# Kernel optimization log

Measured on AMD Instinct MI355X. Metric: run time of the kernel, lower is better.

Reference implementation:

```python
import jax, jax.numpy as jnp
import numpy as np
from itertools import permutations

B, T, J = 65536, 3, 10
W_ASSIGN = 1.0  # assignments_loss_weight
W_CAT = 1.0     # categorizer_loss_weight


def setup_inputs() -> dict:
    key = jax.random.key(0)
    k1, k2, k3, k4 = jax.random.split(key, 4)
    assignments = jax.random.uniform(k1, (B, T, J, J), dtype=jnp.float32)
    category = jax.random.uniform(k2, (B, T), dtype=jnp.float32)
    assignments_labels = jax.random.uniform(k3, (B, T, J, J), dtype=jnp.float32)
    category_labels = jax.random.uniform(k4, (B, T), dtype=jnp.float32)
    return {
        "assignments": assignments,
        "category": category,
        "assignments_labels": assignments_labels,
        "category_labels": category_labels,
    }


def _bce(p, y):
    # torch.nn.BCELoss clamps log terms at -100
    logp = jnp.clip(jnp.log(p), -100.0, None)
    log1mp = jnp.clip(jnp.log1p(-p), -100.0, None)
    return -(y * logp + (1.0 - y) * log1mp)


def reference(assignments, category, assignments_labels, category_labels):
    t = assignments.shape[1]
    perms = jnp.asarray(list(permutations(range(t))), dtype=jnp.int32)  # [P, T]
    # gather all permutations at once: [B, P, T, J, J]
    gathered = assignments[:, perms]
    # per-(event, perm) mean BCE vs labels broadcast over perm axis -> [B, P]
    losses = _bce(gathered, assignments_labels[:, None]).mean(axis=(2, 3, 4))
    batch_losses = losses.min(axis=1)          # [B]
    best = losses.argmin(axis=1)               # [B], first-min tie-break like torch's strict <
    best_perm = perms[best]                    # [B, T]
    permuted_category = jnp.take_along_axis(category, best_perm, axis=1)  # [B, T]
    assignments_loss = batch_losses.mean()
    category_loss = _bce(permuted_category, category_labels).mean()
    return W_ASSIGN * assignments_loss + W_CAT * category_loss
```

## Files before the change

kernel.cpp:

```cpp
#include <hip/hip_runtime.h>


#define CLIP2 (-144.26950408889634f)
#define LN2   (0.6931471805599453f)

__launch_bounds__(256)
__global__ void hybrid_pass1(const float* __restrict__ assign,
                             const float* __restrict__ cat,
                             const float* __restrict__ assign_lab,
                             const float* __restrict__ cat_lab,
                             float* __restrict__ ws, int B) {
    const int tid = blockIdx.x * blockDim.x + threadIdx.x;
    const int b   = tid >> 2;
    const int q   = threadIdx.x & 3;

    float lsum = 0.f;

    if (b < B) {
        const float* Abq = assign     + (size_t)b * 300 + 4 * q;
        const float* Ybq = assign_lab + (size_t)b * 300 + 4 * q;

        const float* cp = cat     + (size_t)b * 3;
        const float* gp = cat_lab + (size_t)b * 3;
        float cb0 = cp[0], cb1 = cp[1], cb2 = cp[2];
        float gb0 = gp[0], gb1 = gp[1], gb2 = gp[2];

        float dacc[3][3] = {{0.f,0.f,0.f},{0.f,0.f,0.f},{0.f,0.f,0.f}};
        float s1a[3]     = {0.f, 0.f, 0.f};

        auto do_chunk = [&](const float* Ap, const float* Yp) {
            float4 av[3], yv[3];
            #pragma unroll
            for (int t = 0; t < 3; ++t) {
                av[t] = *(const float4*)(Ap + t * 100);
                yv[t] = *(const float4*)(Yp + t * 100);
            }
            float d[3][4];
            #pragma unroll
            for (int t = 0; t < 3; ++t) {
                float a[4] = {av[t].x, av[t].y, av[t].z, av[t].w};
                #pragma unroll
                for (int c = 0; c < 4; ++c) {
                    float lp = fmaxf(__log2f(a[c]),        CLIP2);
                    float l1 = fmaxf(__log2f(1.0f - a[c]), CLIP2);
                    d[t][c] = lp - l1;
                    s1a[t] += l1;
                }
            }
            #pragma unroll
            for (int tl = 0; tl < 3; ++tl) {
                float y[4] = {yv[tl].x, yv[tl].y, yv[tl].z, yv[tl].w};
                #pragma unroll
                for (int ta = 0; ta < 3; ++ta) {
                    float acc = dacc[tl][ta];
                    #pragma unroll
                    for (int c = 0; c < 4; ++c)
                        acc = fmaf(y[c], d[ta][c], acc);
                    dacc[tl][ta] = acc;
                }
            }
        };

        #pragma unroll
        for (int k = 0; k < 6; ++k)
            do_chunk(Abq + 16 * k, Ybq + 16 * k);
        if (q == 0)
            do_chunk(Abq + 96, Ybq + 96);

        float e[3][3];
        #pragma unroll
        for (int tl = 0; tl < 3; ++tl)
            #pragma unroll
            for (int ta = 0; ta < 3; ++ta)
                e[tl][ta] = dacc[tl][ta] + s1a[ta];

        #pragma unroll
        for (int off = 1; off <= 2; off <<= 1)
            #pragma unroll
            for (int tl = 0; tl < 3; ++tl)
                #pragma unroll
                for (int ta = 0; ta < 3; ++ta)
                    e[tl][ta] += __shfl_xor(e[tl][ta], off, 64);

        if (q == 0) {
            const int P0[6] = {0,0,1,1,2,2};
            const int P1[6] = {1,2,0,2,0,1};
            const int P2[6] = {2,1,2,0,1,0};
            float best = e[0][0] + e[1][1] + e[2][2];
            int bp0 = 0, bp1 = 1, bp2 = 2;
            #pragma unroll
            for (int p = 1; p < 6; ++p) {
                float l = e[0][P0[p]] + e[1][P1[p]] + e[2][P2[p]];
                if (l > best) { best = l; bp0 = P0[p]; bp1 = P1[p]; bp2 = P2[p]; }
            }

            float lp0 = fmaxf(__log2f(cb0), CLIP2), l10 = fmaxf(__log2f(1.f-cb0), CLIP2);
            float lp1 = fmaxf(__log2f(cb1), CLIP2), l11 = fmaxf(__log2f(1.f-cb1), CLIP2);
            float lp2 = fmaxf(__log2f(cb2), CLIP2), l12 = fmaxf(__log2f(1.f-cb2), CLIP2);

            float lpa = (bp0==0)?lp0:((bp0==1)?lp1:lp2);
            float l1a = (bp0==0)?l10:((bp0==1)?l11:l12);
            float lpb = (bp1==0)?lp0:((bp1==1)?lp1:lp2);
            float l1b = (bp1==0)?l10:((bp1==1)?l11:l12);
            float lpc = (bp2==0)?lp0:((bp2==1)?lp1:lp2);
            float l1c = (bp2==0)?l10:((bp2==1)?l11:l12);

            float csum = -(gb0*lpa + (1.f-gb0)*l1a
                         + gb1*lpb + (1.f-gb1)*l1b
                         + gb2*lpc + (1.f-gb2)*l1c);

            lsum = best * (-1.f/300.f) + csum * (1.f/3.f);
        }
    }

    #pragma unroll
    for (int off = 4; off <= 32; off <<= 1)
        lsum += __shfl_xor(lsum, off, 64);

    __shared__ float sred[4];
    if ((threadIdx.x & 63) == 0) sred[threadIdx.x >> 6] = lsum;
    __syncthreads();
    if (threadIdx.x == 0) {
        float s = (sred[0] + sred[1]) + (sred[2] + sred[3]);
        ws[blockIdx.x] = s * (LN2 / 65536.f);
    }
}

__launch_bounds__(1024)
__global__ void hybrid_pass2(const float* __restrict__ ws,
                             float* __restrict__ out, int n) {
    float s = 0.f;
    for (int i = threadIdx.x; i < n; i += 1024) s += ws[i];
    #pragma unroll
    for (int off = 32; off > 0; off >>= 1) s += __shfl_xor(s, off, 64);
    __shared__ float sm[16];
    if ((threadIdx.x & 63) == 0) sm[threadIdx.x >> 6] = s;
    __syncthreads();
    if (threadIdx.x == 0) {
        float t = 0.f;
        #pragma unroll
        for (int i = 0; i < 16; ++i) t += sm[i];
        out[0] = t;
    }
}

extern "C" void kernel_launch(void* const* d_in, const int* in_sizes, int n_in,
                              void* d_out, int out_size, void* d_ws, size_t ws_size,
                              hipStream_t stream) {
    const float* assign     = (const float*)d_in[0];
    const float* cat        = (const float*)d_in[1];
    const float* assign_lab = (const float*)d_in[2];
    const float* cat_lab    = (const float*)d_in[3];
    float* out = (float*)d_out;
    float* ws  = (float*)d_ws;

    const int B = in_sizes[0] / 300;
    const int blocks = (B * 4 + 255) / 256;

    hybrid_pass1<<<blocks, 256, 0, stream>>>(assign, cat, assign_lab,
                                             cat_lab, ws, B);
    hybrid_pass2<<<1, 1024, 0, stream>>>(ws, out, blocks);
}
```

Baseline: 184.0 us.

## Stage tiles via async global-to-LDS loads with double-buffered persistent blocks

```diff
diff --git a/kernel.cpp b/kernel.cpp
--- a/kernel.cpp
+++ b/kernel.cpp
@@ -1,50 +1,97 @@
 #include <hip/hip_runtime.h>
+#include <stdint.h>
 
 
 #define CLIP2 (-144.26950408889634f)
 #define LN2   (0.6931471805599453f)
 
-__launch_bounds__(256)
+#define TILE_B     8
+#define TILE_F     (TILE_B * 300)
+#define TILE_BYTES (TILE_F * 4)
+#define NCHUNK     10
+
+__device__ __forceinline__ void stage_tile(const float* __restrict__ gA,
+                                           const float* __restrict__ gY,
+                                           float* lA, float* lY,
+                                           int wave, int lane) {
+    for (int c = wave; c < NCHUNK; c += 4) {
+        const int off = c * 1024 + lane * 16;
+        if (off < TILE_BYTES) {
+            __builtin_amdgcn_global_load_lds(
+                (const __attribute__((address_space(1))) uint32_t*)((const char*)gA + off),
+                (__attribute__((address_space(3))) uint32_t*)((char*)lA + c * 1024),
+                16, 0, 0);
+            __builtin_amdgcn_global_load_lds(
+                (const __attribute__((address_space(1))) uint32_t*)((const char*)gY + off),
+                (__attribute__((address_space(3))) uint32_t*)((char*)lY + c * 1024),
+                16, 0, 0);
+        }
+    }
+}
+
+__launch_bounds__(256, 4)
 __global__ void hybrid_pass1(const float* __restrict__ assign,
                              const float* __restrict__ cat,
                              const float* __restrict__ assign_lab,
                              const float* __restrict__ cat_lab,
                              float* __restrict__ ws, int B) {
-    const int tid = blockIdx.x * blockDim.x + threadIdx.x;
-    const int b   = tid >> 2;
-    const int q   = threadIdx.x & 3;
+    __shared__ alignas(16) float lds[2][2][TILE_F];
 
+    const int lane = threadIdx.x & 63;
+    const int wave = threadIdx.x >> 6;
+    const int g    = threadIdx.x >> 5;
+    const int j    = threadIdx.x & 31;
+    const bool act = j < 25;
+
+    const int ntiles = B / TILE_B;
     float lsum = 0.f;
 
-    if (b < B) {
-        const float* Abq = assign     + (size_t)b * 300 + 4 * q;
-        const float* Ybq = assign_lab + (size_t)b * 300 + 4 * q;
+    int t = blockIdx.x;
+    if (t < ntiles)
+        stage_tile(assign + (size_t)t * TILE_F, assign_lab + (size_t)t * TILE_F,
+                   lds[0][0], lds[0][1], wave, lane);
 
-        const float* cp = cat     + (size_t)b * 3;
-        const float* gp = cat_lab + (size_t)b * 3;
-        float cb0 = cp[0], cb1 = cp[1], cb2 = cp[2];
-        float gb0 = gp[0], gb1 = gp[1], gb2 = gp[2];
+    int buf = 0;
+    for (; t < ntiles; t += gridDim.x) {
+        __builtin_amdgcn_s_waitcnt(0x0f70);
+        __syncthreads();
 
-        float dacc[3][3] = {{0.f,0.f,0.f},{0.f,0.f,0.f},{0.f,0.f,0.f}};
-        float s1a[3]     = {0.f, 0.f, 0.f};
+        const int tn = t + gridDim.x;
+        if (tn < ntiles)
+            stage_tile(assign + (size_t)tn * TILE_F,
+                       assign_lab + (size_t)tn * TILE_F,
+                       lds[buf ^ 1][0], lds[buf ^ 1][1], wave, lane);
 
-        auto do_chunk = [&](const float* Ap, const float* Yp) {
+        const int b = t * TILE_B + g;
+
+        float cb0=0.f,cb1=0.f,cb2=0.f,gb0=0.f,gb1=0.f,gb2=0.f;
+        if (j == 0) {
+            const float* cp = cat     + (size_t)b * 3;
+            const float* gp = cat_lab + (size_t)b * 3;
+            cb0 = cp[0]; cb1 = cp[1]; cb2 = cp[2];
+            gb0 = gp[0]; gb1 = gp[1]; gb2 = gp[2];
+        }
+
+        float e[3][3] = {{0.f,0.f,0.f},{0.f,0.f,0.f},{0.f,0.f,0.f}};
+        if (act) {
+            const int f = g * 300 + j * 4;
             float4 av[3], yv[3];
             #pragma unroll
-            for (int t = 0; t < 3; ++t) {
-                av[t] = *(const float4*)(Ap + t * 100);
-                yv[t] = *(const float4*)(Yp + t * 100);
+            for (int tt = 0; tt < 3; ++tt) {
+                av[tt] = *(const float4*)&lds[buf][0][f + tt * 100];
+                yv[tt] = *(const float4*)&lds[buf][1][f + tt * 100];
             }
             float d[3][4];
+            float s1a[3] = {0.f, 0.f, 0.f};
             #pragma unroll
-            for (int t = 0; t < 3; ++t) {
-                float a[4] = {av[t].x, av[t].y, av[t].z, av[t].w};
+            for (int tt = 0; tt < 3; ++tt) {
+                float a[4] = {av[tt].x, av[tt].y, av[tt].z, av[tt].w};
                 #pragma unroll
                 for (int c = 0; c < 4; ++c) {
                     float lp = fmaxf(__log2f(a[c]),        CLIP2);
                     float l1 = fmaxf(__log2f(1.0f - a[c]), CLIP2);
-                    d[t][c] = lp - l1;
-                    s1a[t] += l1;
+                    d[tt][c] = lp - l1;
+                    s1a[tt] += l1;
                 }
             }
             #pragma unroll
@@ -52,37 +99,24 @@
                 float y[4] = {yv[tl].x, yv[tl].y, yv[tl].z, yv[tl].w};
                 #pragma unroll
                 for (int ta = 0; ta < 3; ++ta) {
-                    float acc = dacc[tl][ta];
+                    float acc = s1a[ta];
                     #pragma unroll
                     for (int c = 0; c < 4; ++c)
                         acc = fmaf(y[c], d[ta][c], acc);
-                    dacc[tl][ta] = acc;
+                    e[tl][ta] = acc;
                 }
             }
-        };
+        }
 
         #pragma unroll
-        for (int k = 0; k < 6; ++k)
-            do_chunk(Abq + 16 * k, Ybq + 16 * k);
-        if (q == 0)
-            do_chunk(Abq + 96, Ybq + 96);
-
-        float e[3][3];
-        #pragma unroll
-        for (int tl = 0; tl < 3; ++tl)
-            #pragma unroll
-            for (int ta = 0; ta < 3; ++ta)
-                e[tl][ta] = dacc[tl][ta] + s1a[ta];
-
-        #pragma unroll
-        for (int off = 1; off <= 2; off <<= 1)
+        for (int off = 1; off <= 16; off <<= 1)
             #pragma unroll
             for (int tl = 0; tl < 3; ++tl)
                 #pragma unroll
                 for (int ta = 0; ta < 3; ++ta)
                     e[tl][ta] += __shfl_xor(e[tl][ta], off, 64);
 
-        if (q == 0) {
+        if (j == 0) {
             const int P0[6] = {0,0,1,1,2,2};
             const int P1[6] = {1,2,0,2,0,1};
             const int P2[6] = {2,1,2,0,1,0};
@@ -109,20 +143,18 @@
                          + gb1*lpb + (1.f-gb1)*l1b
                          + gb2*lpc + (1.f-gb2)*l1c);
 
-            lsum = best * (-1.f/300.f) + csum * (1.f/3.f);
+            lsum += best * (-1.f/300.f) + csum * (1.f/3.f);
         }
+        buf ^= 1;
     }
 
-    #pragma unroll
-    for (int off = 4; off <= 32; off <<= 1)
-        lsum += __shfl_xor(lsum, off, 64);
-
+    lsum += __shfl_xor(lsum, 32, 64);
     __shared__ float sred[4];
-    if ((threadIdx.x & 63) == 0) sred[threadIdx.x >> 6] = lsum;
+    if (lane == 0) sred[wave] = lsum;
     __syncthreads();
     if (threadIdx.x == 0) {
         float s = (sred[0] + sred[1]) + (sred[2] + sred[3]);
-        ws[blockIdx.x] = s * (LN2 / 65536.f);
+        ws[blockIdx.x] = s * (LN2 / (float)B);
     }
 }
 
@@ -155,7 +187,7 @@
     float* ws  = (float*)d_ws;
 
     const int B = in_sizes[0] / 300;
-    const int blocks = (B * 4 + 255) / 256;
+    const int blocks = 1024;
 
     hybrid_pass1<<<blocks, 256, 0, stream>>>(assign, cat, assign_lab,
                                              cat_lab, ws, B);
```

Result: no change. 184.6 us (+0.4%).

## Map each event to a 32-lane group with one vector chunk per lane

Applied to the files above, without the earlier changes.

```diff
diff --git a/kernel.cpp b/kernel.cpp
--- a/kernel.cpp
+++ b/kernel.cpp
@@ -3,6 +3,8 @@
 
 #define CLIP2 (-144.26950408889634f)
 #define LN2   (0.6931471805599453f)
+
+typedef float vfloat4 __attribute__((ext_vector_type(4)));
 
 __launch_bounds__(256)
 __global__ void hybrid_pass1(const float* __restrict__ assign,
@@ -10,119 +12,104 @@
                              const float* __restrict__ assign_lab,
                              const float* __restrict__ cat_lab,
                              float* __restrict__ ws, int B) {
-    const int tid = blockIdx.x * blockDim.x + threadIdx.x;
-    const int b   = tid >> 2;
-    const int q   = threadIdx.x & 3;
+    const int sub = threadIdx.x & 31;
+    const int b   = (blockIdx.x * blockDim.x + threadIdx.x) >> 5;
+    if (b >= B) return;
 
-    float lsum = 0.f;
+    const bool act = sub < 25;
+    float e[3][3] = {{0.f,0.f,0.f},{0.f,0.f,0.f},{0.f,0.f,0.f}};
 
-    if (b < B) {
-        const float* Abq = assign     + (size_t)b * 300 + 4 * q;
-        const float* Ybq = assign_lab + (size_t)b * 300 + 4 * q;
+    if (act) {
+        const vfloat4* Ab = (const vfloat4*)(assign     + (size_t)b * 300 + sub * 4);
+        const vfloat4* Yb = (const vfloat4*)(assign_lab + (size_t)b * 300 + sub * 4);
+        vfloat4 av[3], yv[3];
+        #pragma unroll
+        for (int t = 0; t < 3; ++t) {
+            av[t] = __builtin_nontemporal_load(Ab + t * 25);
+            yv[t] = __builtin_nontemporal_load(Yb + t * 25);
+        }
 
+        float d[3][4];
+        float s1p[3] = {0.f, 0.f, 0.f};
+        #pragma unroll
+        for (int t = 0; t < 3; ++t) {
+            #pragma unroll
+            for (int c = 0; c < 4; ++c) {
+                float a  = av[t][c];
+                float lp = fmaxf(__log2f(a),        CLIP2);
+                float l1 = fmaxf(__log2f(1.0f - a), CLIP2);
+                d[t][c] = lp - l1;
+                s1p[t] += l1;
+            }
+        }
+        #pragma unroll
+        for (int tl = 0; tl < 3; ++tl) {
+            #pragma unroll
+            for (int ta = 0; ta < 3; ++ta) {
+                float acc = s1p[ta];
+                #pragma unroll
+                for (int c = 0; c < 4; ++c)
+                    acc = fmaf(yv[tl][c], d[ta][c], acc);
+                e[tl][ta] = acc;
+            }
+        }
+    }
+
+    float cb0=0.f,cb1=0.f,cb2=0.f,gb0=0.f,gb1=0.f,gb2=0.f;
+    if (sub == 0) {
         const float* cp = cat     + (size_t)b * 3;
         const float* gp = cat_lab + (size_t)b * 3;
-        float cb0 = cp[0], cb1 = cp[1], cb2 = cp[2];
-        float gb0 = gp[0], gb1 = gp[1], gb2 = gp[2];
+        cb0 = cp[0]; cb1 = cp[1]; cb2 = cp[2];
+        gb0 = gp[0]; gb1 = gp[1]; gb2 = gp[2];
+    }
 
-        float dacc[3][3] = {{0.f,0.f,0.f},{0.f,0.f,0.f},{0.f,0.f,0.f}};
-        float s1a[3]     = {0.f, 0.f, 0.f};
-
-        auto do_chunk = [&](const float* Ap, const float* Yp) {
-            float4 av[3], yv[3];
-            #pragma unroll
-            for (int t = 0; t < 3; ++t) {
-                av[t] = *(const float4*)(Ap + t * 100);
-                yv[t] = *(const float4*)(Yp + t * 100);
-            }
-            float d[3][4];
-            #pragma unroll
-            for (int t = 0; t < 3; ++t) {
-                float a[4] = {av[t].x, av[t].y, av[t].z, av[t].w};
-                #pragma unroll
-                for (int c = 0; c < 4; ++c) {
-                    float lp = fmaxf(__log2f(a[c]),        CLIP2);
-                    float l1 = fmaxf(__log2f(1.0f - a[c]), CLIP2);
-                    d[t][c] = lp - l1;
-                    s1a[t] += l1;
-                }
-            }
-            #pragma unroll
-            for (int tl = 0; tl < 3; ++tl) {
-                float y[4] = {yv[tl].x, yv[tl].y, yv[tl].z, yv[tl].w};
-                #pragma unroll
-                for (int ta = 0; ta < 3; ++ta) {
-                    float acc = dacc[tl][ta];
-                    #pragma unroll
-                    for (int c = 0; c < 4; ++c)
-                        acc = fmaf(y[c], d[ta][c], acc);
-                    dacc[tl][ta] = acc;
-                }
-            }
-        };
-
-        #pragma unroll
-        for (int k = 0; k < 6; ++k)
-            do_chunk(Abq + 16 * k, Ybq + 16 * k);
-        if (q == 0)
-            do_chunk(Abq + 96, Ybq + 96);
-
-        float e[3][3];
+    #pragma unroll
+    for (int off = 1; off <= 16; off <<= 1)
         #pragma unroll
         for (int tl = 0; tl < 3; ++tl)
             #pragma unroll
             for (int ta = 0; ta < 3; ++ta)
-                e[tl][ta] = dacc[tl][ta] + s1a[ta];
+                e[tl][ta] += __shfl_xor(e[tl][ta], off, 64);
 
+    float lsum = 0.f;
+    if (sub == 0) {
+        const int P0[6] = {0,0,1,1,2,2};
+        const int P1[6] = {1,2,0,2,0,1};
+        const int P2[6] = {2,1,2,0,1,0};
+        float best = e[0][0] + e[1][1] + e[2][2];
+        int bp0 = 0, bp1 = 1, bp2 = 2;
         #pragma unroll
-        for (int off = 1; off <= 2; off <<= 1)
-            #pragma unroll
-            for (int tl = 0; tl < 3; ++tl)
-                #pragma unroll
-                for (int ta = 0; ta < 3; ++ta)
-                    e[tl][ta] += __shfl_xor(e[tl][ta], off, 64);
+        for (int p = 1; p < 6; ++p) {
+            float l = e[0][P0[p]] + e[1][P1[p]] + e[2][P2[p]];
+            if (l > best) { best = l; bp0 = P0[p]; bp1 = P1[p]; bp2 = P2[p]; }
+        }
 
-        if (q == 0) {
-            const int P0[6] = {0,0,1,1,2,2};
-            const int P1[6] = {1,2,0,2,0,1};
-            const int P2[6] = {2,1,2,0,1,0};
-            float best = e[0][0] + e[1][1] + e[2][2];
-            int bp0 = 0, bp1 = 1, bp2 = 2;
-            #pragma unroll
-            for (int p = 1; p < 6; ++p) {
-                float l = e[0][P0[p]] + e[1][P1[p]] + e[2][P2[p]];
-                if (l > best) { best = l; bp0 = P0[p]; bp1 = P1[p]; bp2 = P2[p]; }
-            }
+        float lp0 = fmaxf(__log2f(cb0), CLIP2), l10 = fmaxf(__log2f(1.f-cb0), CLIP2);
+        float lp1 = fmaxf(__log2f(cb1), CLIP2), l11 = fmaxf(__log2f(1.f-cb1), CLIP2);
+        float lp2 = fmaxf(__log2f(cb2), CLIP2), l12 = fmaxf(__log2f(1.f-cb2), CLIP2);
 
-            float lp0 = fmaxf(__log2f(cb0), CLIP2), l10 = fmaxf(__log2f(1.f-cb0), CLIP2);
-            float lp1 = fmaxf(__log2f(cb1), CLIP2), l11 = fmaxf(__log2f(1.f-cb1), CLIP2);
-            float lp2 = fmaxf(__log2f(cb2), CLIP2), l12 = fmaxf(__log2f(1.f-cb2), CLIP2);
+        float lpa = (bp0==0)?lp0:((bp0==1)?lp1:lp2);
+        float l1a = (bp0==0)?l10:((bp0==1)?l11:l12);
+        float lpb = (bp1==0)?lp0:((bp1==1)?lp1:lp2);
+        float l1b = (bp1==0)?l10:((bp1==1)?l11:l12);
+        float lpc = (bp2==0)?lp0:((bp2==1)?lp1:lp2);
+        float l1c = (bp2==0)?l10:((bp2==1)?l11:l12);
 
-            float lpa = (bp0==0)?lp0:((bp0==1)?lp1:lp2);
-            float l1a = (bp0==0)?l10:((bp0==1)?l11:l12);
-            float lpb = (bp1==0)?lp0:((bp1==1)?lp1:lp2);
-            float l1b = (bp1==0)?l10:((bp1==1)?l11:l12);
-            float lpc = (bp2==0)?lp0:((bp2==1)?lp1:lp2);
-            float l1c = (bp2==0)?l10:((bp2==1)?l11:l12);
+        float csum = -(gb0*lpa + (1.f-gb0)*l1a
+                     + gb1*lpb + (1.f-gb1)*l1b
+                     + gb2*lpc + (1.f-gb2)*l1c);
 
-            float csum = -(gb0*lpa + (1.f-gb0)*l1a
-                         + gb1*lpb + (1.f-gb1)*l1b
-                         + gb2*lpc + (1.f-gb2)*l1c);
-
-            lsum = best * (-1.f/300.f) + csum * (1.f/3.f);
-        }
+        lsum = best * (-1.f/300.f) + csum * (1.f/3.f);
     }
 
-    #pragma unroll
-    for (int off = 4; off <= 32; off <<= 1)
-        lsum += __shfl_xor(lsum, off, 64);
-
-    __shared__ float sred[4];
-    if ((threadIdx.x & 63) == 0) sred[threadIdx.x >> 6] = lsum;
+    __shared__ float sred[8];
+    if (sub == 0) sred[threadIdx.x >> 5] = lsum;
     __syncthreads();
     if (threadIdx.x == 0) {
-        float s = (sred[0] + sred[1]) + (sred[2] + sred[3]);
-        ws[blockIdx.x] = s * (LN2 / 65536.f);
+        float s = 0.f;
+        #pragma unroll
+        for (int i = 0; i < 8; ++i) s += sred[i];
+        ws[blockIdx.x] = s * (LN2 / (float)B);
     }
 }
 
@@ -155,7 +142,7 @@
     float* ws  = (float*)d_ws;
 
     const int B = in_sizes[0] / 300;
-    const int blocks = (B * 4 + 255) / 256;
+    const int blocks = (B * 32 + 255) / 256;
 
     hybrid_pass1<<<blocks, 256, 0, stream>>>(assign, cat, assign_lab,
                                              cat_lab, ws, B);
```

New measurement: 165.1 us, median of 2. -10.2%, faster.
